# Optimization experiments

Hardware: AMD Instinct MI355X
Metric: run time of the kernel (lower is better)

The kernel has to match this reference:

```python
import jax, jax.numpy as jnp
import numpy as np
import math

EMBED_DIM = 1024
NUM_HEADS = 16
B, S = 4, 4096
NEG_INF = -1e30


def setup_inputs() -> dict:
    key = jax.random.key(0)
    k1, k2, k3, k4 = jax.random.split(key, 4)
    D = EMBED_DIM
    # xavier_uniform bounds
    lim_in = math.sqrt(6.0 / (3 * D + D))
    lim_out = math.sqrt(6.0 / (D + D))
    return {
        "x": jax.random.normal(k1, (B, S, D), dtype=jnp.float32),
        "in_proj_weight": jax.random.uniform(k2, (3 * D, D), dtype=jnp.float32, minval=-lim_in, maxval=lim_in),
        "in_proj_bias": jnp.zeros((3 * D,), dtype=jnp.float32),
        "out_proj_weight": jax.random.uniform(k3, (D, D), dtype=jnp.float32, minval=-lim_out, maxval=lim_out),
        "out_proj_bias": jnp.zeros((D,), dtype=jnp.float32),
    }


def _cron_root_attention(q, k, v):
    """Causal sqrt(N) block-sparse attention.

    q,k,v: [B, H, S, hd]. Sequence split into nb blocks of size b = sqrt(S).
    Each query attends to: (a) keys in its own block (causal within block),
    (b) one summary key per strictly-previous block (the block's last key).
    Complexity O(S * (b + nb)) = O(N * sqrt(N)).
    """
    Bq, H, Sq, hd = q.shape
    b = int(round(math.sqrt(Sq)))
    nb = Sq // b
    scale = 1.0 / math.sqrt(hd)

    qb = q.reshape(Bq, H, nb, b, hd)
    kb = k.reshape(Bq, H, nb, b, hd)
    vb = v.reshape(Bq, H, nb, b, hd)
    ks = k[:, :, b - 1::b, :]  # [B, H, nb, hd] summary keys (last of each block)
    vs = v[:, :, b - 1::b, :]

    # local (within-block) scores, causal mask
    s_loc = jnp.einsum("bhnqd,bhnkd->bhnqk", qb, kb) * scale  # [B,H,nb,b,b]
    idx = jnp.arange(b)
    loc_mask = idx[:, None] >= idx[None, :]  # [b, b]
    s_loc = jnp.where(loc_mask[None, None, None], s_loc, NEG_INF)

    # strided scores to summary keys of strictly previous blocks
    s_str = jnp.einsum("bhnqd,bhmd->bhnqm", qb, ks) * scale  # [B,H,nb,b,nb]
    nidx = jnp.arange(nb)
    str_mask = nidx[:, None] > nidx[None, :]  # [nb(query block), nb(key block)]
    s_str = jnp.where(str_mask[None, None, :, None, :], s_str, NEG_INF)

    # joint softmax over local + strided keys
    scores = jnp.concatenate([s_loc, s_str], axis=-1)  # [B,H,nb,b,b+nb]
    w = jax.nn.softmax(scores, axis=-1)
    w_loc, w_str = w[..., :b], w[..., b:]

    out = jnp.einsum("bhnqk,bhnkd->bhnqd", w_loc, vb) \
        + jnp.einsum("bhnqm,bhmd->bhnqd", w_str, vs)
    return out.reshape(Bq, H, Sq, hd)


def reference(x, in_proj_weight, in_proj_bias, out_proj_weight, out_proj_bias):
    Bx, Sx, D = x.shape
    H = NUM_HEADS
    hd = D // H
    qkv = x @ in_proj_weight.T + in_proj_bias  # [B,S,3D]
    qkv = jnp.transpose(qkv.reshape(Bx, Sx, 3, H, hd), (2, 0, 3, 1, 4))
    q, k, v = qkv[0], qkv[1], qkv[2]  # each [B,H,S,hd]
    out = _cron_root_attention(q, k, v)  # [B,H,S,hd]
    out = jnp.transpose(out, (0, 2, 1, 3)).reshape(Bx, Sx, D)
    return out @ out_proj_weight.T + out_proj_bias
```

## Files before the change

### kernel.cpp

```cpp
#include <hip/hip_runtime.h>
#include <stdint.h>

typedef __attribute__((ext_vector_type(8))) short short8;
typedef __attribute__((ext_vector_type(4))) float f32x4;
typedef __attribute__((ext_vector_type(4))) float f4;
typedef __attribute__((ext_vector_type(4))) ushort us4;

#define AS1 __attribute__((address_space(1)))
#define AS3 __attribute__((address_space(3)))

__device__ __forceinline__ ushort f2bf(float f) {
  uint u = __builtin_bit_cast(uint, f);
  u += 0x7fffu + ((u >> 16) & 1u);
  return (ushort)(u >> 16);
}

__global__ void cvt_bf16(const float* __restrict__ in, ushort* __restrict__ out, int n4) {
  int i = blockIdx.x * blockDim.x + threadIdx.x;
  int stride = gridDim.x * blockDim.x;
  for (; i < n4; i += stride) {
    f4 v = ((const f4*)in)[i];
    us4 o;
    o[0] = f2bf(v[0]); o[1] = f2bf(v[1]); o[2] = f2bf(v[2]); o[3] = f2bf(v[3]);
    ((us4*)out)[i] = o;
  }
}


__device__ __forceinline__ void stage_tile(const ushort* __restrict__ gbase, int row0,
                                           int pitch, int k0, char* lds, int tid) {
#pragma unroll
  for (int i = 0; i < 4; ++i) {
    uint chunk = i * 256 + tid;
    uint Q = chunk << 4;
    uint L = Q ^ (((Q >> 7) & 7u) << 4);
    uint row = L >> 7;
    uint kb = L & 127u;
    const char* g = (const char*)(gbase + (size_t)(row0 + (int)row) * pitch + k0) + kb;
    char* l = lds + (size_t)((i * 256 + (tid & ~63)) << 4);
    __builtin_amdgcn_global_load_lds((const AS1 void*)g, (AS3 void*)l, 16, 0, 0);
  }
}

template <int OUT_F32>
__global__ __launch_bounds__(256) void gemm_bt(const ushort* __restrict__ A,
                                               const ushort* __restrict__ Bw,
                                               const float* __restrict__ bias,
                                               void* __restrict__ Cout,
                                               int M, int N, int K) {
  __shared__ char sA[16384];
  __shared__ char sB[16384];
  int tid = threadIdx.x;
  int nbn = N >> 7;
  int bm = blockIdx.x / nbn, bn = blockIdx.x % nbn;
  int lane = tid & 63, l15 = lane & 15, lk = lane >> 4;
  int w = tid >> 6;
  int wr = w >> 1, wc = w & 1;

  f32x4 acc[4][4];
  f32x4 zero = {0.f, 0.f, 0.f, 0.f};
#pragma unroll
  for (int i = 0; i < 4; ++i)
#pragma unroll
    for (int j = 0; j < 4; ++j) acc[i][j] = zero;

  for (int k0 = 0; k0 < K; k0 += 64) {
    stage_tile(A, bm * 128, K, k0, sA, tid);
    stage_tile(Bw, bn * 128, K, k0, sB, tid);
    __syncthreads();

    short8 af[4][2], bf[4][2];
#pragma unroll
    for (int mt = 0; mt < 4; ++mt)
#pragma unroll
      for (int kk = 0; kk < 2; ++kk) {
        uint rowa = wr * 64 + mt * 16 + l15;
        uint ba = (rowa << 7) + (kk << 6) + (lk << 4);
        af[mt][kk] = *(const short8*)&sA[ba ^ ((rowa & 7u) << 4)];
        uint rowb = wc * 64 + mt * 16 + l15;
        uint bb = (rowb << 7) + (kk << 6) + (lk << 4);
        bf[mt][kk] = *(const short8*)&sB[bb ^ ((rowb & 7u) << 4)];
      }
#pragma unroll
    for (int kk = 0; kk < 2; ++kk)
#pragma unroll
      for (int mt = 0; mt < 4; ++mt)
#pragma unroll
        for (int nt = 0; nt < 4; ++nt)
          acc[mt][nt] = __builtin_amdgcn_mfma_f32_16x16x32_bf16(af[mt][kk], bf[nt][kk],
                                                                acc[mt][nt], 0, 0, 0);
    __syncthreads();
  }

#pragma unroll
  for (int mt = 0; mt < 4; ++mt)
#pragma unroll
    for (int nt = 0; nt < 4; ++nt)
#pragma unroll
      for (int r = 0; r < 4; ++r) {
        int row = bm * 128 + wr * 64 + mt * 16 + lk * 4 + r;
        int col = bn * 128 + wc * 64 + nt * 16 + l15;
        float v = acc[mt][nt][r] + bias[col];
        if constexpr (OUT_F32)
          ((float*)Cout)[(size_t)row * N + col] = v;
        else
          ((ushort*)Cout)[(size_t)row * N + col] = f2bf(v);
      }
}

__global__ __launch_bounds__(256) void cron_attn(const ushort* __restrict__ qkv,
                                                 ushort* __restrict__ aout) {
  const int S = 4096, CQ = 3072;
  int bid = blockIdx.x;
  int n = bid & 63;
  int h = (bid >> 6) & 15;
  int b = bid >> 10;
  int tid = threadIdx.x;
  int w = tid >> 6, lane = tid & 63, l15 = lane & 15, lk = lane >> 4;

  const ushort* qp = qkv + (size_t)b * S * CQ + h * 64;
  const ushort* kp = qp + 1024;
  const ushort* vp = qp + 2048;

  __shared__ char vT[16384];
  __shared__ char pL[4][4096];

  {
    int r = tid >> 1;
    int half = tid & 1;
    int srow = (r < 64) ? (n * 64 + r) : ((r - 64) * 64 + 63);
    const ushort* src = vp + (size_t)srow * CQ + half * 32;
    short8 vv0 = ((const short8*)src)[0];
    short8 vv1 = ((const short8*)src)[1];
    short8 vv2 = ((const short8*)src)[2];
    short8 vv3 = ((const short8*)src)[3];
#pragma unroll
    for (int j = 0; j < 8; ++j) {
      int d0 = half * 32 + j;
      *(short*)&vT[(uint)(d0 * 256 + r * 2) ^ (((uint)d0 & 7u) << 4)] = vv0[j];
      int d1 = half * 32 + 8 + j;
      *(short*)&vT[(uint)(d1 * 256 + r * 2) ^ (((uint)d1 & 7u) << 4)] = vv1[j];
      int d2 = half * 32 + 16 + j;
      *(short*)&vT[(uint)(d2 * 256 + r * 2) ^ (((uint)d2 & 7u) << 4)] = vv2[j];
      int d3 = half * 32 + 24 + j;
      *(short*)&vT[(uint)(d3 * 256 + r * 2) ^ (((uint)d3 & 7u) << 4)] = vv3[j];
    }
  }
  __syncthreads();

  short8 aq[2];
  {
    int srow = n * 64 + w * 16 + l15;
#pragma unroll
    for (int kk = 0; kk < 2; ++kk)
      aq[kk] = *(const short8*)(qp + (size_t)srow * CQ + kk * 32 + lk * 8);
  }

  f32x4 sc[8];
  f32x4 zero = {0.f, 0.f, 0.f, 0.f};
#pragma unroll
  for (int c = 0; c < 8; ++c) sc[c] = zero;
#pragma unroll
  for (int c = 0; c < 8; ++c) {
    int key = (c < 4) ? (n * 64 + c * 16 + l15) : (((c - 4) * 16 + l15) * 64 + 63);
    const ushort* kr = kp + (size_t)key * CQ;
#pragma unroll
    for (int kk = 0; kk < 2; ++kk) {
      short8 bk = *(const short8*)(kr + kk * 32 + lk * 8);
      sc[c] = __builtin_amdgcn_mfma_f32_16x16x32_bf16(aq[kk], bk, sc[c], 0, 0, 0);
    }
  }

  float p[8][4];
  int qrow = w * 16 + lk * 4;
#pragma unroll
  for (int c = 0; c < 8; ++c)
#pragma unroll
    for (int r = 0; r < 4; ++r) {
      float s = sc[c][r] * 0.125f;
      bool ok = (c < 4) ? ((qrow + r) >= (c * 16 + l15)) : (((c - 4) * 16 + l15) < n);
      p[c][r] = ok ? s : -1e30f;
    }

#pragma unroll
  for (int r = 0; r < 4; ++r) {
    float m = p[0][r];
#pragma unroll
    for (int c = 1; c < 8; ++c) m = fmaxf(m, p[c][r]);
    m = fmaxf(m, __shfl_xor(m, 1));
    m = fmaxf(m, __shfl_xor(m, 2));
    m = fmaxf(m, __shfl_xor(m, 4));
    m = fmaxf(m, __shfl_xor(m, 8));
    float sum = 0.f;
#pragma unroll
    for (int c = 0; c < 8; ++c) {
      p[c][r] = __expf(p[c][r] - m);
      sum += p[c][r];
    }
    sum += __shfl_xor(sum, 1);
    sum += __shfl_xor(sum, 2);
    sum += __shfl_xor(sum, 4);
    sum += __shfl_xor(sum, 8);
    float rs = 1.f / sum;
#pragma unroll
    for (int c = 0; c < 8; ++c) p[c][r] *= rs;
  }

  char* myP = pL[w];
#pragma unroll
  for (int c = 0; c < 8; ++c)
#pragma unroll
    for (int r = 0; r < 4; ++r) {
      uint row = lk * 4 + r;
      uint byte = row * 256 + (c * 16 + l15) * 2;
      *(short*)&myP[byte ^ ((row & 7u) << 4)] = (short)f2bf(p[c][r]);
    }
  short8 ap[4];
#pragma unroll
  for (int kk = 0; kk < 4; ++kk) {
    uint row = (uint)l15;
    uint byte = row * 256 + (kk * 32 + lk * 8) * 2;
    ap[kk] = *(const short8*)&myP[byte ^ ((row & 7u) << 4)];
  }

  f32x4 ao[4];
#pragma unroll
  for (int dc = 0; dc < 4; ++dc) ao[dc] = zero;
#pragma unroll
  for (int dc = 0; dc < 4; ++dc)
#pragma unroll
    for (int kk = 0; kk < 4; ++kk) {
      uint d = dc * 16 + l15;
      uint byte = d * 256 + (kk * 32 + lk * 8) * 2;
      short8 bv = *(const short8*)&vT[byte ^ ((d & 7u) << 4)];
      ao[dc] = __builtin_amdgcn_mfma_f32_16x16x32_bf16(ap[kk], bv, ao[dc], 0, 0, 0);
    }

#pragma unroll
  for (int dc = 0; dc < 4; ++dc)
#pragma unroll
    for (int r = 0; r < 4; ++r) {
      int srow = n * 64 + w * 16 + lk * 4 + r;
      int col = h * 64 + dc * 16 + l15;
      aout[((size_t)(b * S + srow)) * 1024 + col] = f2bf(ao[dc][r]);
    }
}

extern "C" void kernel_launch(void* const* d_in, const int* in_sizes, int n_in,
                              void* d_out, int out_size, void* d_ws, size_t ws_size,
                              hipStream_t stream) {
  const float* x = (const float*)d_in[0];
  const float* wi = (const float*)d_in[1];
  const float* bi = (const float*)d_in[2];
  const float* wo = (const float*)d_in[3];
  const float* bo = (const float*)d_in[4];
  float* out = (float*)d_out;
  char* ws = (char*)d_ws;

  ushort* xb = (ushort*)(ws);
  ushort* wib = (ushort*)(ws + (size_t)33554432);
  ushort* wob = (ushort*)(ws + (size_t)39845888);
  ushort* qkvb = (ushort*)(ws + (size_t)41943040);
  ushort* aob = (ushort*)(ws + (size_t)142606336);

  cvt_bf16<<<2048, 256, 0, stream>>>(x, xb, (16384 * 1024) / 4);
  cvt_bf16<<<768, 256, 0, stream>>>(wi, wib, (3072 * 1024) / 4);
  cvt_bf16<<<256, 256, 0, stream>>>(wo, wob, (1024 * 1024) / 4);

  gemm_bt<0><<<128 * 24, 256, 0, stream>>>(xb, wib, bi, qkvb, 16384, 3072, 1024);
  cron_attn<<<4096, 256, 0, stream>>>(qkvb, aob);
  gemm_bt<1><<<128 * 8, 256, 0, stream>>>(aob, wob, bo, out, 16384, 1024, 1024);
}
```

Baseline: 262.7 us.

## Replace GEMM with 256x256-tile double-buffered pipelined kernel and grid swizzle

```diff
diff --git a/kernel.cpp b/kernel.cpp
--- a/kernel.cpp
+++ b/kernel.cpp
@@ -27,80 +27,121 @@
 }
 
 
-__device__ __forceinline__ void stage_tile(const ushort* __restrict__ gbase, int row0,
-                                           int pitch, int k0, char* lds, int tid) {
-#pragma unroll
-  for (int i = 0; i < 4; ++i) {
-    uint chunk = i * 256 + tid;
+__device__ __forceinline__ void stage_half(const ushort* __restrict__ g, int pitch,
+                                           int row0, int k0, char* ldsbase, int tid) {
+#pragma unroll
+  for (int i = 0; i < 2; ++i) {
+    uint chunk = i * 512 + tid;
     uint Q = chunk << 4;
     uint L = Q ^ (((Q >> 7) & 7u) << 4);
     uint row = L >> 7;
     uint kb = L & 127u;
-    const char* g = (const char*)(gbase + (size_t)(row0 + (int)row) * pitch + k0) + kb;
-    char* l = lds + (size_t)((i * 256 + (tid & ~63)) << 4);
-    __builtin_amdgcn_global_load_lds((const AS1 void*)g, (AS3 void*)l, 16, 0, 0);
-  }
+    const char* gp = (const char*)(g + (size_t)(row0 + (int)row) * pitch + k0) + kb;
+    char* lp = ldsbase + ((i * 512 + (tid & ~63)) << 4);
+    __builtin_amdgcn_global_load_lds((const AS1 void*)gp, (AS3 void*)lp, 16, 0, 0);
+  }
+}
+
+__device__ __forceinline__ void stage_j(int j, const ushort* __restrict__ A,
+                                        const ushort* __restrict__ Bw, int K,
+                                        int arow0, int brow0, char* sA, char* sB, int tid) {
+  int t = j >> 2, h = j & 3;
+  int k0 = t << 6;
+  char* base = ((h < 2) ? sB : sA) + ((t & 1) << 15) + ((h & 1) << 14);
+  const ushort* g = (h < 2) ? Bw : A;
+  int row0 = ((h < 2) ? brow0 : arow0) + ((h & 1) << 7);
+  stage_half(g, K, row0, k0, base, tid);
 }
 
 template <int OUT_F32>
-__global__ __launch_bounds__(256) void gemm_bt(const ushort* __restrict__ A,
-                                               const ushort* __restrict__ Bw,
-                                               const float* __restrict__ bias,
-                                               void* __restrict__ Cout,
-                                               int M, int N, int K) {
-  __shared__ char sA[16384];
-  __shared__ char sB[16384];
-  int tid = threadIdx.x;
-  int nbn = N >> 7;
-  int bm = blockIdx.x / nbn, bn = blockIdx.x % nbn;
-  int lane = tid & 63, l15 = lane & 15, lk = lane >> 4;
-  int w = tid >> 6;
-  int wr = w >> 1, wc = w & 1;
-
-  f32x4 acc[4][4];
+__global__ __launch_bounds__(512, 1) void gemm256(const ushort* __restrict__ A,
+                                                  const ushort* __restrict__ Bw,
+                                                  const float* __restrict__ bias,
+                                                  void* __restrict__ Cout,
+                                                  int M, int N, int K, int gn) {
+  __shared__ char sA[65536];
+  __shared__ char sB[65536];
+  const int tid = threadIdx.x;
+  const int lane = tid & 63, l15 = lane & 15, lk = lane >> 4;
+  const int w = tid >> 6;
+  const int wm = w >> 2, wn = w & 3;
+  const int NT = K >> 6;
+
+  int q8 = gridDim.x >> 3;
+  int bid = blockIdx.x;
+  int swz = (bid & 7) * q8 + (bid >> 3);
+  int bm = swz / gn, bn = swz % gn;
+  const int arow0 = bm << 8, brow0 = bn << 8;
+
+  f32x4 acc[8][4];
   f32x4 zero = {0.f, 0.f, 0.f, 0.f};
 #pragma unroll
-  for (int i = 0; i < 4; ++i)
+  for (int i = 0; i < 8; ++i)
 #pragma unroll
     for (int j = 0; j < 4; ++j) acc[i][j] = zero;
 
-  for (int k0 = 0; k0 < K; k0 += 64) {
-    stage_tile(A, bm * 128, K, k0, sA, tid);
-    stage_tile(Bw, bn * 128, K, k0, sB, tid);
-    __syncthreads();
-
-    short8 af[4][2], bf[4][2];
-#pragma unroll
-    for (int mt = 0; mt < 4; ++mt)
-#pragma unroll
-      for (int kk = 0; kk < 2; ++kk) {
-        uint rowa = wr * 64 + mt * 16 + l15;
-        uint ba = (rowa << 7) + (kk << 6) + (lk << 4);
-        af[mt][kk] = *(const short8*)&sA[ba ^ ((rowa & 7u) << 4)];
-        uint rowb = wc * 64 + mt * 16 + l15;
-        uint bb = (rowb << 7) + (kk << 6) + (lk << 4);
-        bf[mt][kk] = *(const short8*)&sB[bb ^ ((rowb & 7u) << 4)];
+#pragma unroll
+  for (int j = 0; j < 7; ++j)
+    if (j < 4 * NT) stage_j(j, A, Bw, K, arow0, brow0, sA, sB, tid);
+  asm volatile("s_waitcnt vmcnt(6)" ::: "memory");
+  __builtin_amdgcn_s_barrier();
+
+  for (int t = 0; t < NT; ++t) {
+    const char* bA = sA + ((t & 1) << 15);
+    const char* bB = sB + ((t & 1) << 15);
+    short8 bfr[4][2];
+#pragma unroll
+    for (int qd = 0; qd < 4; ++qd) {
+      short8 afr[2][2];
+      if (qd == 0) {
+#pragma unroll
+        for (int ni = 0; ni < 4; ++ni)
+#pragma unroll
+          for (int kk = 0; kk < 2; ++kk) {
+            uint row = (uint)(wn * 64 + ni * 16 + l15);
+            uint byte = (row << 7) + (kk << 6) + (lk << 4);
+            bfr[ni][kk] = *(const short8*)&bB[byte ^ ((row & 7u) << 4)];
+          }
       }
 #pragma unroll
-    for (int kk = 0; kk < 2; ++kk)
-#pragma unroll
-      for (int mt = 0; mt < 4; ++mt)
-#pragma unroll
-        for (int nt = 0; nt < 4; ++nt)
-          acc[mt][nt] = __builtin_amdgcn_mfma_f32_16x16x32_bf16(af[mt][kk], bf[nt][kk],
-                                                                acc[mt][nt], 0, 0, 0);
-    __syncthreads();
-  }
-
-#pragma unroll
-  for (int mt = 0; mt < 4; ++mt)
-#pragma unroll
-    for (int nt = 0; nt < 4; ++nt)
+      for (int mi = 0; mi < 2; ++mi)
+#pragma unroll
+        for (int kk = 0; kk < 2; ++kk) {
+          uint row = (uint)(wm * 128 + (qd * 2 + mi) * 16 + l15);
+          uint byte = (row << 7) + (kk << 6) + (lk << 4);
+          afr[mi][kk] = *(const short8*)&bA[byte ^ ((row & 7u) << 4)];
+        }
+      int j = 4 * t + qd + 7;
+      if (j < 4 * NT) stage_j(j, A, Bw, K, arow0, brow0, sA, sB, tid);
+      if (qd == 3) {
+        if (t < NT - 2) asm volatile("s_waitcnt vmcnt(6)" ::: "memory");
+        else if (t == NT - 2) asm volatile("s_waitcnt vmcnt(0)" ::: "memory");
+      }
+      __builtin_amdgcn_s_barrier();
+      asm volatile("s_waitcnt lgkmcnt(0)" ::: "memory");
+      __builtin_amdgcn_s_setprio(1);
+#pragma unroll
+      for (int kk = 0; kk < 2; ++kk)
+#pragma unroll
+        for (int mi = 0; mi < 2; ++mi)
+#pragma unroll
+          for (int ni = 0; ni < 4; ++ni)
+            acc[qd * 2 + mi][ni] = __builtin_amdgcn_mfma_f32_16x16x32_bf16(
+                afr[mi][kk], bfr[ni][kk], acc[qd * 2 + mi][ni], 0, 0, 0);
+      __builtin_amdgcn_s_setprio(0);
+      __builtin_amdgcn_s_barrier();
+    }
+  }
+
+#pragma unroll
+  for (int m = 0; m < 8; ++m)
+#pragma unroll
+    for (int ni = 0; ni < 4; ++ni)
 #pragma unroll
       for (int r = 0; r < 4; ++r) {
-        int row = bm * 128 + wr * 64 + mt * 16 + lk * 4 + r;
-        int col = bn * 128 + wc * 64 + nt * 16 + l15;
-        float v = acc[mt][nt][r] + bias[col];
+        int row = arow0 + wm * 128 + m * 16 + lk * 4 + r;
+        int col = brow0 + wn * 64 + ni * 16 + l15;
+        float v = acc[m][ni][r] + bias[col];
         if constexpr (OUT_F32)
           ((float*)Cout)[(size_t)row * N + col] = v;
         else
@@ -267,7 +308,7 @@
   cvt_bf16<<<768, 256, 0, stream>>>(wi, wib, (3072 * 1024) / 4);
   cvt_bf16<<<256, 256, 0, stream>>>(wo, wob, (1024 * 1024) / 4);
 
-  gemm_bt<0><<<128 * 24, 256, 0, stream>>>(xb, wib, bi, qkvb, 16384, 3072, 1024);
+  gemm256<0><<<64 * 12, 512, 0, stream>>>(xb, wib, bi, qkvb, 16384, 3072, 1024, 12);
   cron_attn<<<4096, 256, 0, stream>>>(qkvb, aob);
-  gemm_bt<1><<<128 * 8, 256, 0, stream>>>(aob, wob, bo, out, 16384, 1024, 1024);
-}
+  gemm256<1><<<64 * 4, 512, 0, stream>>>(aob, wob, bo, out, 16384, 1024, 1024, 4);
+}
```

New measurement: 225.1 us. -14.3%, faster.
